# Performance work log

Hardware: AMD Instinct MI355X
Metric: run time of the kernel (lower is better)

The kernel has to match this reference:

```python
import jax, jax.numpy as jnp
import numpy as np

R = 512      # latent dim
M = 4        # center dimensionality
L = 256      # number of cluster centers
B = 8192     # batch
SIGMA_EPS = 1e-4


def setup_inputs() -> dict:
    key = jax.random.key(0)
    kx, kc = jax.random.split(key)
    x = jax.random.normal(kx, (B, R), dtype=jnp.float32)
    c = jax.random.normal(kc, (M, L), dtype=jnp.float32)   # codebook centers
    sigma = jnp.full((1,), 5.0, dtype=jnp.float32)         # trainable temperature
    return {"x": x, "c": c, "sigma": sigma}


def reference(x, c, sigma):
    b = x.shape[0]
    nf = R // M
    z = x.reshape(b, nf, M)                                # (b, nf, m)
    sig = jax.nn.relu(sigma[0]) + SIGMA_EPS
    # squared distances ||z - c||^2 over m, expanded to avoid (b,nf,m,L) materialization
    z_sq = jnp.sum(z * z, axis=-1, keepdims=True)          # (b, nf, 1)
    c_sq = jnp.sum(c * c, axis=0)                          # (L,)
    zc = jnp.einsum('bnm,ml->bnl', z, c)                   # (b, nf, L)
    dist = z_sq - 2.0 * zc + c_sq[None, None, :]           # (b, nf, L)
    q = jax.nn.softmax(-sig * dist, axis=-1)               # soft assignments (b, nf, L)
    out = jnp.einsum('bnl,ml->bnm', q, c)                  # weighted centers (b, nf, m)
    return out.reshape(b, R)
```

## Files before the change

kernel.cpp:

```cpp
#include <hip/hip_runtime.h>
#include <math.h>

#define RDIM 512
#define MDIM 4
#define LDIM 256
#define BDIM 8192
#define NROWS (BDIM * (RDIM / MDIM))
#define SIGMA_EPS 1e-4f
#define LOG2E 1.4426950408889634f
#define SHIFT_HEADROOM 96.0f

typedef _Float16 half4_t __attribute__((ext_vector_type(4)));
typedef short    short8_t __attribute__((ext_vector_type(8)));
typedef __fp16   fp16x2_t __attribute__((ext_vector_type(2)));
typedef float    float4_t __attribute__((ext_vector_type(4)));

#define NRT (NROWS / 16)
#define MAIN_BLOCKS 2048
#define WPB 4
#define NT (NRT / (MAIN_BLOCKS * WPB))
#define QUAD 2

static __device__ __host__ inline unsigned short bf16_rne(float f) {
  unsigned u = __builtin_bit_cast(unsigned, f);
  return (unsigned short)((u + 0x7FFFu + ((u >> 16) & 1u)) >> 16);
}

__global__ void prep_kernel(const float* __restrict__ c, const float* __restrict__ sigma,
                            _Float16* __restrict__ a1w, unsigned short* __restrict__ a2w) {
  const int gid  = blockIdx.x * 256 + threadIdx.x;
  const int lane = gid & 63;
  const int q4   = lane >> 4;
  const int m    = lane & 15;
  const float sig   = fmaxf(sigma[0], 0.0f) + SIGMA_EPS;
  const float sigL  = sig * LOG2E;
  const float sig2L = 2.0f * sigL;
  if (gid < 1024) {
    const int t = gid >> 6;
    const int l = t * 16 + m;
    float cv[4];
    cv[0] = c[l]; cv[1] = c[256 + l]; cv[2] = c[512 + l]; cv[3] = c[768 + l];
    _Float16 uh[4], ul[4];
    #pragma unroll
    for (int i = 0; i < 4; ++i) {
      float u = sig2L * cv[i];
      uh[i] = (_Float16)u;
      ul[i] = (_Float16)(u - (float)uh[i]);
    }
    float bias = -sigL * fmaf(cv[0], cv[0], fmaf(cv[1], cv[1], fmaf(cv[2], cv[2], cv[3] * cv[3])));
    _Float16 bh = (_Float16)bias;
    _Float16 bl = (_Float16)(bias - (float)bh);
    #pragma unroll
    for (int j = 0; j < 4; ++j) {
      _Float16 v;
      if      (q4 <  2) v = uh[j];
      else if (q4 == 2) v = ul[j];
      else              v = (j == 0) ? bh : ((j == 1) ? bl : (_Float16)1.0f);
      a1w[(t * 64 + lane) * 4 + j] = v;
    }
  } else if (gid < 1536) {
    const int p = (gid - 1024) >> 6;
    #pragma unroll
    for (int j = 0; j < 8; ++j) {
      int center = 32 * p + 16 * (j >> 2) + 4 * q4 + (j & 3);
      unsigned short v = 0;
      if (m < 4)       v = bf16_rne(c[m * 256 + center]);
      else if (m == 4) v = (unsigned short)0x3F80;
      a2w[(p * 64 + lane) * 8 + j] = v;
    }
  }
}

union U2H4 { uint2 u; half4_t h; };
union U4S8 { uint4 u; short8_t s; };

static __device__ __forceinline__ U2H4 make_b1(const float4& z, float sigL, int q4,
                                               unsigned one_one) {
  fp16x2_t zh01 = __builtin_amdgcn_cvt_pkrtz(z.x, z.y);
  fp16x2_t zh23 = __builtin_amdgcn_cvt_pkrtz(z.z, z.w);
  fp16x2_t zl01 = __builtin_amdgcn_cvt_pkrtz(z.x - (float)zh01[0], z.y - (float)zh01[1]);
  fp16x2_t zl23 = __builtin_amdgcn_cvt_pkrtz(z.z - (float)zh23[0], z.w - (float)zh23[1]);
  const unsigned zh01u = __builtin_bit_cast(unsigned, zh01);
  const unsigned zh23u = __builtin_bit_cast(unsigned, zh23);
  const unsigned zl01u = __builtin_bit_cast(unsigned, zl01);
  const unsigned zl23u = __builtin_bit_cast(unsigned, zl23);
  float U = sigL * fmaf(z.x, z.x, fmaf(z.y, z.y, fmaf(z.z, z.z, z.w * z.w))) - SHIFT_HEADROOM;
  float Uh = (float)(_Float16)U;
  fp16x2_t nU = __builtin_amdgcn_cvt_pkrtz(-Uh, -(U - Uh));
  const unsigned w0 = (q4 == 1) ? zl01u : ((q4 == 3) ? one_one : zh01u);
  const unsigned w1 = (q4 == 3) ? __builtin_bit_cast(unsigned, nU)
                                : ((q4 == 1) ? zl23u : zh23u);
  U2H4 b1; b1.u = make_uint2(w0, w1);
  return b1;
}

__global__ __launch_bounds__(256, 4) void sq_mfma_kernel(
    const float4* __restrict__ x4,
    const _Float16* __restrict__ a1w,
    const unsigned short* __restrict__ a2w,
    const float* __restrict__ sigma,
    float4* __restrict__ out4) {
  const int tid  = threadIdx.x;
  const int lane = tid & 63;
  const int q4   = lane >> 4;
  const int zr   = lane & 15;

  __shared__ __align__(16) short8_t a2s[8 * 64];

  {
    const short8_t* a2p = (const short8_t*)a2w;
    a2s[tid]       = a2p[tid];
    a2s[tid + 256] = a2p[tid + 256];
  }

  const float sigL = (fmaxf(sigma[0], 0.0f) + SIGMA_EPS) * LOG2E;

  half4_t a1[16];
  const half4_t* a1p = (const half4_t*)a1w;
  #pragma unroll
  for (int t = 0; t < 16; ++t) a1[t] = a1p[t * 64 + lane];

  __syncthreads();

  const int gw = blockIdx.x * WPB + (tid >> 6);
  const int tilebase = gw * NT;
  const float4_t zero4 = {0.f, 0.f, 0.f, 0.f};
  const unsigned one_one = 0x3C003C00u;

  float4 zq[QUAD];
  #pragma unroll
  for (int ch = 0; ch < QUAD; ++ch) zq[ch] = x4[(tilebase + ch) * 16 + zr];

  for (int it = 0; it < NT; it += QUAD) {
    const int itn = (it + QUAD < NT) ? (it + QUAD) : it;
    float4 zn[QUAD];
    #pragma unroll
    for (int ch = 0; ch < QUAD; ++ch) zn[ch] = x4[(tilebase + itn + ch) * 16 + zr];

    U2H4 b1[QUAD];
    #pragma unroll
    for (int ch = 0; ch < QUAD; ++ch) b1[ch] = make_b1(zq[ch], sigL, q4, one_one);

    float4_t d2[QUAD];
    #pragma unroll
    for (int ch = 0; ch < QUAD; ++ch) d2[ch] = zero4;

    #pragma unroll
    for (int p = 0; p < 8; ++p) {
      const short8_t a2f = a2s[p * 64 + lane];
      float4_t sa[QUAD], sb[QUAD];
      #pragma unroll
      for (int ch = 0; ch < QUAD; ++ch) {
        sa[ch] = __builtin_amdgcn_mfma_f32_16x16x16f16(a1[2 * p],     b1[ch].h, zero4, 0, 0, 0);
        sb[ch] = __builtin_amdgcn_mfma_f32_16x16x16f16(a1[2 * p + 1], b1[ch].h, zero4, 0, 0, 0);
      }
      #pragma unroll
      for (int ch = 0; ch < QUAD; ++ch) {
        float e0 = __builtin_amdgcn_exp2f(sa[ch][0]);
        float e1 = __builtin_amdgcn_exp2f(sa[ch][1]);
        float e2 = __builtin_amdgcn_exp2f(sa[ch][2]);
        float e3 = __builtin_amdgcn_exp2f(sa[ch][3]);
        float e4 = __builtin_amdgcn_exp2f(sb[ch][0]);
        float e5 = __builtin_amdgcn_exp2f(sb[ch][1]);
        float e6 = __builtin_amdgcn_exp2f(sb[ch][2]);
        float e7 = __builtin_amdgcn_exp2f(sb[ch][3]);
        U4S8 b2;
        b2.u.x = __builtin_amdgcn_perm(__builtin_bit_cast(unsigned, e1),
                                       __builtin_bit_cast(unsigned, e0), 0x07060302u);
        b2.u.y = __builtin_amdgcn_perm(__builtin_bit_cast(unsigned, e3),
                                       __builtin_bit_cast(unsigned, e2), 0x07060302u);
        b2.u.z = __builtin_amdgcn_perm(__builtin_bit_cast(unsigned, e5),
                                       __builtin_bit_cast(unsigned, e4), 0x07060302u);
        b2.u.w = __builtin_amdgcn_perm(__builtin_bit_cast(unsigned, e7),
                                       __builtin_bit_cast(unsigned, e6), 0x07060302u);
        d2[ch] = __builtin_amdgcn_mfma_f32_16x16x32_bf16(a2f, b2.s, d2[ch], 0, 0, 0);
      }
    }

    float den[QUAD];
    #pragma unroll
    for (int ch = 0; ch < QUAD; ++ch) den[ch] = __shfl(d2[ch][0], zr + 16);
    if (lane < 16) {
      #pragma unroll
      for (int ch = 0; ch < QUAD; ++ch) {
        float r = __builtin_amdgcn_rcpf(den[ch]);
        out4[(tilebase + it + ch) * 16 + zr] =
            make_float4(d2[ch][0] * r, d2[ch][1] * r, d2[ch][2] * r, d2[ch][3] * r);
      }
    }

    #pragma unroll
    for (int ch = 0; ch < QUAD; ++ch) zq[ch] = zn[ch];
  }
}

extern "C" void kernel_launch(void* const* d_in, const int* in_sizes, int n_in,
                              void* d_out, int out_size, void* d_ws, size_t ws_size,
                              hipStream_t stream) {
  const float4* x4    = (const float4*)d_in[0];
  const float*  c     = (const float*)d_in[1];
  const float*  sigma = (const float*)d_in[2];
  float4*       out4  = (float4*)d_out;

  _Float16*       a1w = (_Float16*)d_ws;
  unsigned short* a2w = (unsigned short*)(a1w + 16 * 64 * 4);

  prep_kernel<<<6, 256, 0, stream>>>(c, sigma, a1w, a2w);
  sq_mfma_kernel<<<MAIN_BLOCKS, 256, 0, stream>>>(x4, a1w, a2w, sigma, out4);
}
```

Before: 98.02 us.

## Fuse codebook prep into main kernel and stage A-operands in LDS

Removes the separate prep kernel launch: every block now builds the fp16 split distance operand and the bf16 center operand from c and sigma directly into shared memory. The distance-matrix A fragments are read from LDS inside the loop instead of being held in 16 registers, which frees registers so the launch bound rises to 5 waves per SIMD. The grid doubles to 4096 blocks, each handling half as many tiles. The cost is redundant per-block recomputation of the codebook tables and extra LDS reads in the inner loop.

```diff
diff --git a/kernel.cpp b/kernel.cpp
--- a/kernel.cpp
+++ b/kernel.cpp
@@ -16,59 +16,14 @@
 typedef float    float4_t __attribute__((ext_vector_type(4)));
 
 #define NRT (NROWS / 16)
-#define MAIN_BLOCKS 2048
+#define MAIN_BLOCKS 4096
 #define WPB 4
 #define NT (NRT / (MAIN_BLOCKS * WPB))
 #define QUAD 2
 
-static __device__ __host__ inline unsigned short bf16_rne(float f) {
+static __device__ inline unsigned short bf16_rne(float f) {
   unsigned u = __builtin_bit_cast(unsigned, f);
   return (unsigned short)((u + 0x7FFFu + ((u >> 16) & 1u)) >> 16);
-}
-
-__global__ void prep_kernel(const float* __restrict__ c, const float* __restrict__ sigma,
-                            _Float16* __restrict__ a1w, unsigned short* __restrict__ a2w) {
-  const int gid  = blockIdx.x * 256 + threadIdx.x;
-  const int lane = gid & 63;
-  const int q4   = lane >> 4;
-  const int m    = lane & 15;
-  const float sig   = fmaxf(sigma[0], 0.0f) + SIGMA_EPS;
-  const float sigL  = sig * LOG2E;
-  const float sig2L = 2.0f * sigL;
-  if (gid < 1024) {
-    const int t = gid >> 6;
-    const int l = t * 16 + m;
-    float cv[4];
-    cv[0] = c[l]; cv[1] = c[256 + l]; cv[2] = c[512 + l]; cv[3] = c[768 + l];
-    _Float16 uh[4], ul[4];
-    #pragma unroll
-    for (int i = 0; i < 4; ++i) {
-      float u = sig2L * cv[i];
-      uh[i] = (_Float16)u;
-      ul[i] = (_Float16)(u - (float)uh[i]);
-    }
-    float bias = -sigL * fmaf(cv[0], cv[0], fmaf(cv[1], cv[1], fmaf(cv[2], cv[2], cv[3] * cv[3])));
-    _Float16 bh = (_Float16)bias;
-    _Float16 bl = (_Float16)(bias - (float)bh);
-    #pragma unroll
-    for (int j = 0; j < 4; ++j) {
-      _Float16 v;
-      if      (q4 <  2) v = uh[j];
-      else if (q4 == 2) v = ul[j];
-      else              v = (j == 0) ? bh : ((j == 1) ? bl : (_Float16)1.0f);
-      a1w[(t * 64 + lane) * 4 + j] = v;
-    }
-  } else if (gid < 1536) {
-    const int p = (gid - 1024) >> 6;
-    #pragma unroll
-    for (int j = 0; j < 8; ++j) {
-      int center = 32 * p + 16 * (j >> 2) + 4 * q4 + (j & 3);
-      unsigned short v = 0;
-      if (m < 4)       v = bf16_rne(c[m * 256 + center]);
-      else if (m == 4) v = (unsigned short)0x3F80;
-      a2w[(p * 64 + lane) * 8 + j] = v;
-    }
-  }
 }
 
 union U2H4 { uint2 u; half4_t h; };
@@ -94,32 +49,71 @@
   return b1;
 }
 
-__global__ __launch_bounds__(256, 4) void sq_mfma_kernel(
+__global__ __launch_bounds__(256, 5) void sq_fused_kernel(
     const float4* __restrict__ x4,
-    const _Float16* __restrict__ a1w,
-    const unsigned short* __restrict__ a2w,
-    const float* __restrict__ sigma,
-    float4* __restrict__ out4) {
+    const float*  __restrict__ c,
+    const float*  __restrict__ sigma,
+    float4*       __restrict__ out4) {
   const int tid  = threadIdx.x;
   const int lane = tid & 63;
   const int q4   = lane >> 4;
   const int zr   = lane & 15;
 
+  __shared__ __align__(16) half4_t  a1s[16 * 64];
   __shared__ __align__(16) short8_t a2s[8 * 64];
 
-  {
-    const short8_t* a2p = (const short8_t*)a2w;
-    a2s[tid]       = a2p[tid];
-    a2s[tid + 256] = a2p[tid + 256];
+  const float sig   = fmaxf(sigma[0], 0.0f) + SIGMA_EPS;
+  const float sigL  = sig * LOG2E;
+  const float sig2L = 2.0f * sigL;
+
+  #pragma unroll
+  for (int w = 0; w < 4; ++w) {
+    const int s  = w * 256 + tid;
+    const int t  = s >> 6;
+    const int ls = s & 63;
+    const int qs = ls >> 4;
+    const int ms = ls & 15;
+    const int l  = t * 16 + ms;
+    float c0 = c[l], c1 = c[256 + l], c2 = c[512 + l], c3 = c[768 + l];
+    float bias = -sigL * fmaf(c0, c0, fmaf(c1, c1, fmaf(c2, c2, c3 * c3)));
+    half4_t v;
+    if (qs < 3) {
+      float u0 = sig2L * c0, u1 = sig2L * c1, u2 = sig2L * c2, u3 = sig2L * c3;
+      if (qs < 2) {
+        v[0] = (_Float16)u0; v[1] = (_Float16)u1; v[2] = (_Float16)u2; v[3] = (_Float16)u3;
+      } else {
+        _Float16 h0 = (_Float16)u0, h1 = (_Float16)u1, h2 = (_Float16)u2, h3 = (_Float16)u3;
+        v[0] = (_Float16)(u0 - (float)h0); v[1] = (_Float16)(u1 - (float)h1);
+        v[2] = (_Float16)(u2 - (float)h2); v[3] = (_Float16)(u3 - (float)h3);
+      }
+    } else {
+      _Float16 bh = (_Float16)bias;
+      v[0] = bh; v[1] = (_Float16)(bias - (float)bh);
+      v[2] = (_Float16)1.0f; v[3] = (_Float16)1.0f;
+    }
+    a1s[t * 64 + ls] = v;
   }
-
-  const float sigL = (fmaxf(sigma[0], 0.0f) + SIGMA_EPS) * LOG2E;
-
-  half4_t a1[16];
-  const half4_t* a1p = (const half4_t*)a1w;
   #pragma unroll
-  for (int t = 0; t < 16; ++t) a1[t] = a1p[t * 64 + lane];
-
+  for (int w = 0; w < 2; ++w) {
+    const int s  = w * 256 + tid;
+    const int p  = s >> 6;
+    const int ls = s & 63;
+    const int qs = ls >> 4;
+    const int ms = ls & 15;
+    unsigned short e[8];
+    #pragma unroll
+    for (int j = 0; j < 8; ++j) {
+      int center = 32 * p + 16 * (j >> 2) + 4 * qs + (j & 3);
+      unsigned short vv = 0;
+      if (ms < 4)       vv = bf16_rne(c[ms * 256 + center]);
+      else if (ms == 4) vv = (unsigned short)0x3F80;
+      e[j] = vv;
+    }
+    short8_t v8;
+    #pragma unroll
+    for (int j = 0; j < 8; ++j) v8[j] = (short)e[j];
+    a2s[p * 64 + ls] = v8;
+  }
   __syncthreads();
 
   const int gw = blockIdx.x * WPB + (tid >> 6);
@@ -147,12 +141,14 @@
 
     #pragma unroll
     for (int p = 0; p < 8; ++p) {
+      const half4_t  a1a = a1s[(2 * p) * 64 + lane];
+      const half4_t  a1b = a1s[(2 * p + 1) * 64 + lane];
       const short8_t a2f = a2s[p * 64 + lane];
       float4_t sa[QUAD], sb[QUAD];
       #pragma unroll
       for (int ch = 0; ch < QUAD; ++ch) {
-        sa[ch] = __builtin_amdgcn_mfma_f32_16x16x16f16(a1[2 * p],     b1[ch].h, zero4, 0, 0, 0);
-        sb[ch] = __builtin_amdgcn_mfma_f32_16x16x16f16(a1[2 * p + 1], b1[ch].h, zero4, 0, 0, 0);
+        sa[ch] = __builtin_amdgcn_mfma_f32_16x16x16f16(a1a, b1[ch].h, zero4, 0, 0, 0);
+        sb[ch] = __builtin_amdgcn_mfma_f32_16x16x16f16(a1b, b1[ch].h, zero4, 0, 0, 0);
       }
       #pragma unroll
       for (int ch = 0; ch < QUAD; ++ch) {
@@ -201,10 +197,7 @@
   const float*  c     = (const float*)d_in[1];
   const float*  sigma = (const float*)d_in[2];
   float4*       out4  = (float4*)d_out;
-
-  _Float16*       a1w = (_Float16*)d_ws;
-  unsigned short* a2w = (unsigned short*)(a1w + 16 * 64 * 4);
-
-  prep_kernel<<<6, 256, 0, stream>>>(c, sigma, a1w, a2w);
-  sq_mfma_kernel<<<MAIN_BLOCKS, 256, 0, stream>>>(x4, a1w, a2w, sigma, out4);
-}
+  (void)d_ws; (void)ws_size;
+
+  sq_fused_kernel<<<MAIN_BLOCKS, 256, 0, stream>>>(x4, c, sigma, out4);
+}
```

New measurement: 101.6 us. +3.6%, slower.
